# Kernel optimization log

Hardware: AMD Instinct MI355X
Metric: run time of the kernel (lower is better)

## Reference

```python
import jax, jax.numpy as jnp
import numpy as np

B, F, N = 128, 256, 2000

def setup_inputs() -> dict:
    key = jax.random.key(0)
    ks = jax.random.split(key, 10)
    s = 0.05
    return {
        'nfeature': jax.random.normal(ks[0], (B, F, N, 1), jnp.float32),
        'last_current': jax.random.randint(ks[1], (B, 2), 0, N, jnp.int32),
        'Wg': jax.random.normal(ks[2], (F, F), jnp.float32) * s,
        'bg': jax.random.normal(ks[3], (F,), jnp.float32) * s,
        'Wnode': jax.random.normal(ks[4], (3 * F, F), jnp.float32) * s,
        'bnode': jax.random.normal(ks[5], (3 * F,), jnp.float32) * s,
        'Wlc': jax.random.normal(ks[6], (F, 2 * F), jnp.float32) * s,
        'blc': jax.random.normal(ks[7], (F,), jnp.float32) * s,
        'Wproj': jax.random.normal(ks[8], (F, F), jnp.float32) * s,
        'bproj': jax.random.normal(ks[9], (F,), jnp.float32) * s,
    }

def reference(nfeature, last_current, Wg, bg, Wnode, bnode, Wlc, blc, Wproj, bproj):
    # nfeature: [B, F, N, 1]
    x = nfeature[..., 0]                                  # [B, F, N]
    f = x.shape[1]
    scale = 1.0 / jnp.sqrt(jnp.asarray(f, x.dtype))
    # global fixed query: max over nodes then Linear
    glb = jnp.max(x, axis=2)                              # [B, F]
    Q = glb @ Wg.T + bg                                   # [B, F]
    # node embeddings via 1x1 conv == channel GEMM, split into K, V, logit_K
    kvl = jnp.einsum('bfn,gf->bgn', x, Wnode) + bnode[None, :, None]  # [B, 3F, N]
    K, V, Klog = jnp.split(kvl, 3, axis=1)                # each [B, F, N]
    # gather last/current city features
    lc = jnp.take_along_axis(x, last_current[:, None, :], axis=2)     # [B, F, 2]
    context = jnp.concatenate([lc[:, :, 0], lc[:, :, 1]], axis=1)     # [B, 2F]
    cQ = context @ Wlc.T + blc + Q                        # [B, F]
    # attention: single query over N keys
    ucj = jnp.einsum('bf,bfn->bn', cQ, K) * scale         # [B, N]
    attn = jax.nn.softmax(ucj, axis=1)
    nc = jnp.einsum('bn,bfn->bf', attn, V)                # [B, F]
    nc = nc @ Wproj.T + bproj                             # [B, F]
    logits = jnp.einsum('bf,bfn->bn', nc, Klog) * scale   # [B, N]
    return jnp.tanh(logits) * 10.0
```

## Files before the change

### kernel.cpp

```cpp
#include <hip/hip_runtime.h>
#include <hip/hip_fp16.h>
#include <math.h>

#define BB 128
#define FF 256
#define NN 2000

typedef float f32x4 __attribute__((ext_vector_type(4)));
union H8 { f32x4 v; __half2 h[4]; };

__global__ __launch_bounds__(256) void k_convmax(const float* __restrict__ x,
                                                 __half* __restrict__ xh,
                                                 float* __restrict__ glb) {
    int row  = (blockIdx.x << 2) | (threadIdx.x >> 6);
    int lane = threadIdx.x & 63;
    const f32x4* src = (const f32x4*)(x + (size_t)row * NN);
    f32x4*       dst = (f32x4*)(xh + (size_t)row * NN);
    float m = -INFINITY;
    for (int i = lane; i < 250; i += 64) {
        f32x4 a = __builtin_nontemporal_load(src + 2 * i);
        f32x4 b = __builtin_nontemporal_load(src + 2 * i + 1);
        m = fmaxf(m, fmaxf(fmaxf(a.x, a.y), fmaxf(a.z, a.w)));
        m = fmaxf(m, fmaxf(fmaxf(b.x, b.y), fmaxf(b.z, b.w)));
        H8 o;
        o.h[0] = __floats2half2_rn(a.x, a.y);
        o.h[1] = __floats2half2_rn(a.z, a.w);
        o.h[2] = __floats2half2_rn(b.x, b.y);
        o.h[3] = __floats2half2_rn(b.z, b.w);
        dst[i] = o.v;
    }
#pragma unroll
    for (int off = 32; off; off >>= 1) m = fmaxf(m, __shfl_xor(m, off));
    if (!lane) glb[row] = m;
}

__global__ __launch_bounds__(256) void k_prep(
    const float* __restrict__ x, const int* __restrict__ lc,
    const float* __restrict__ glb,
    const float* __restrict__ Wg, const float* __restrict__ bg,
    const float* __restrict__ Wnode, const float* __restrict__ bnode,
    const float* __restrict__ Wlc, const float* __restrict__ blc,
    float* __restrict__ cK, float* __restrict__ cK0)
{
    int b = blockIdx.x;
    int f = threadIdx.x;
    __shared__ float s_glb[FF], s_ctx[2 * FF], s_cQ[FF], s_red[FF];
    const float* xb = x + (size_t)b * FF * NN;
    s_glb[f] = glb[b * FF + f];
    int l0 = lc[2 * b], l1 = lc[2 * b + 1];
    s_ctx[f]      = xb[(size_t)f * NN + l0];
    s_ctx[FF + f] = xb[(size_t)f * NN + l1];
    __syncthreads();
    const float* wg = Wg + (size_t)f * FF;
    float q0 = 0, q1 = 0, q2 = 0, q3 = 0;
    for (int j = 0; j < FF; j += 4) {
        q0 = fmaf(wg[j],     s_glb[j],     q0);
        q1 = fmaf(wg[j + 1], s_glb[j + 1], q1);
        q2 = fmaf(wg[j + 2], s_glb[j + 2], q2);
        q3 = fmaf(wg[j + 3], s_glb[j + 3], q3);
    }
    const float* wl = Wlc + (size_t)f * 2 * FF;
    for (int j = 0; j < 2 * FF; j += 4) {
        q0 = fmaf(wl[j],     s_ctx[j],     q0);
        q1 = fmaf(wl[j + 1], s_ctx[j + 1], q1);
        q2 = fmaf(wl[j + 2], s_ctx[j + 2], q2);
        q3 = fmaf(wl[j + 3], s_ctx[j + 3], q3);
    }
    float cq = bg[f] + blc[f] + ((q0 + q1) + (q2 + q3));
    s_cQ[f]  = cq;
    s_red[f] = cq * bnode[f];
    __syncthreads();
    float c0 = 0, c1 = 0;
    for (int g = 0; g < FF; g += 2) {
        c0 = fmaf(s_cQ[g],     Wnode[(size_t)g * FF + f],       c0);
        c1 = fmaf(s_cQ[g + 1], Wnode[(size_t)(g + 1) * FF + f], c1);
    }
    cK[b * FF + f] = c0 + c1;
    for (int s = 128; s > 0; s >>= 1) {
        if (f < s) s_red[f] += s_red[f + s];
        __syncthreads();
    }
    if (f == 0) cK0[b] = s_red[0];
}

__global__ __launch_bounds__(512) void k_attn(
    const __half* __restrict__ xh,
    const float* __restrict__ cK, const float* __restrict__ cK0,
    float* __restrict__ y_part8, float* __restrict__ m_part,
    float* __restrict__ s_part)
{
    int b = blockIdx.x >> 2, s = blockIdx.x & 3;
    int tid = threadIdx.x, w = tid >> 6, lane = tid & 63;
    __shared__ float s_cK[FF];
    __shared__ float s_buf[8][512];
    __shared__ float s_p[512];
    __shared__ float s_red[8], s_red2[8];
    if (tid < FF) s_cK[tid] = cK[b * FF + tid];
    __syncthreads();

    int n0 = s << 9;
    int nbase = n0 + (lane << 3);
    bool valid = nbase < NN;
    int cb = lane << 3;
    const __half* rp = xh + (size_t)(b * FF + (w << 5)) * NN + nbase;

    float a0 = 0, a1 = 0, a2 = 0, a3 = 0, a4 = 0, a5 = 0, a6 = 0, a7 = 0;
    if (valid) {
#pragma unroll
        for (int g = 0; g < 4; ++g) {
            f32x4 hv[8];
#pragma unroll
            for (int r = 0; r < 8; ++r)
                hv[r] = *(const f32x4*)(rp + (size_t)((g << 3) + r) * NN);
#pragma unroll
            for (int r = 0; r < 8; ++r) {
                H8 u; u.v = hv[r];
                float c = s_cK[(w << 5) + (g << 3) + r];
                float2 q0 = __half22float2(u.h[0]);
                float2 q1 = __half22float2(u.h[1]);
                float2 q2 = __half22float2(u.h[2]);
                float2 q3 = __half22float2(u.h[3]);
                a0 = fmaf(c, q0.x, a0); a1 = fmaf(c, q0.y, a1);
                a2 = fmaf(c, q1.x, a2); a3 = fmaf(c, q1.y, a3);
                a4 = fmaf(c, q2.x, a4); a5 = fmaf(c, q2.y, a5);
                a6 = fmaf(c, q3.x, a6); a7 = fmaf(c, q3.y, a7);
            }
        }
    }
    s_buf[w][cb + 0] = a0; s_buf[w][cb + 1] = a1;
    s_buf[w][cb + 2] = a2; s_buf[w][cb + 3] = a3;
    s_buf[w][cb + 4] = a4; s_buf[w][cb + 5] = a5;
    s_buf[w][cb + 6] = a6; s_buf[w][cb + 7] = a7;
    __syncthreads();

    const float scale = 0.0625f;
    float k0 = cK0[b];
    float u = 0.f;
#pragma unroll
    for (int ww = 0; ww < 8; ++ww) u += s_buf[ww][tid];
    float uu = (n0 + tid < NN) ? (u + k0) * scale : -INFINITY;
    float m = uu;
#pragma unroll
    for (int off = 32; off; off >>= 1) m = fmaxf(m, __shfl_xor(m, off));
    if (!lane) s_red[w] = m;
    __syncthreads();
    float M = s_red[0];
#pragma unroll
    for (int ww = 1; ww < 8; ++ww) M = fmaxf(M, s_red[ww]);
    float e = (uu > -INFINITY) ? __expf(uu - M) : 0.f;
    s_p[tid] = e;
    float ss = e;
#pragma unroll
    for (int off = 32; off; off >>= 1) ss += __shfl_xor(ss, off);
    if (!lane) s_red2[w] = ss;
    __syncthreads();
    if (!tid) {
        float S = 0.f;
#pragma unroll
        for (int ww = 0; ww < 8; ++ww) S += s_red2[ww];
        m_part[(b << 2) + s] = M;
        s_part[(b << 2) + s] = S;
    }

    float4 pa = *(const float4*)&s_p[cb];
    float4 pc = *(const float4*)&s_p[cb + 4];
    float* yout = y_part8 + (size_t)((b << 2) + s) * 2048 + (w << 8);
    int row = lane >> 3, k = lane & 7;
#pragma unroll
    for (int g = 0; g < 4; ++g) {
        float part[8];
#pragma unroll
        for (int r = 0; r < 8; ++r) {
            float acc = 0.f;
            if (valid) {
                H8 u2; u2.v = *(const f32x4*)(rp + (size_t)((g << 3) + r) * NN);
                float2 q0 = __half22float2(u2.h[0]);
                float2 q1 = __half22float2(u2.h[1]);
                float2 q2 = __half22float2(u2.h[2]);
                float2 q3 = __half22float2(u2.h[3]);
                acc = fmaf(pa.x, q0.x, acc); acc = fmaf(pa.y, q0.y, acc);
                acc = fmaf(pa.z, q1.x, acc); acc = fmaf(pa.w, q1.y, acc);
                acc = fmaf(pc.x, q2.x, acc); acc = fmaf(pc.y, q2.y, acc);
                acc = fmaf(pc.z, q3.x, acc); acc = fmaf(pc.w, q3.y, acc);
            }
            part[r] = acc;
        }
#pragma unroll
        for (int r = 0; r < 8; ++r) s_buf[w][(r << 6) + lane] = part[r];
        const float* srcp = &s_buf[w][(row << 6) + (k << 3)];
        float4 aa = *(const float4*)srcp;
        float4 bb = *(const float4*)(srcp + 4);
        yout[(g << 6) + lane] =
            ((aa.x + aa.y) + (aa.z + aa.w)) + ((bb.x + bb.y) + (bb.z + bb.w));
    }
}

__global__ __launch_bounds__(256) void k_dense(
    const float* __restrict__ y_part8, const float* __restrict__ m_part,
    const float* __restrict__ s_part,
    const float* __restrict__ Wnode, const float* __restrict__ bnode,
    const float* __restrict__ Wproj, const float* __restrict__ bproj,
    float* __restrict__ cL, float* __restrict__ cL0)
{
    int b = blockIdx.x;
    int f = threadIdx.x;
    int wid = f >> 6, lane = f & 63;
    __shared__ float s_y[FF], s_v[FF], s_red[4];

    float m0 = m_part[(b << 2)],     m1 = m_part[(b << 2) + 1];
    float m2 = m_part[(b << 2) + 2], m3 = m_part[(b << 2) + 3];
    float M = fmaxf(fmaxf(m0, m1), fmaxf(m2, m3));
    float w0 = __expf(m0 - M), w1 = __expf(m1 - M);
    float w2 = __expf(m2 - M), w3 = __expf(m3 - M);
    float S = s_part[(b << 2)] * w0 + s_part[(b << 2) + 1] * w1 +
              s_part[(b << 2) + 2] * w2 + s_part[(b << 2) + 3] * w3;
    float invS = 1.0f / S;
    const float* yb = y_part8 + ((size_t)b << 13);
    float wgt[4] = {w0, w1, w2, w3};
    float acc = 0.f;
#pragma unroll
    for (int s = 0; s < 4; ++s) {
        float4 aa = *(const float4*)(yb + (s << 11) + (f << 3));
        float4 bb = *(const float4*)(yb + (s << 11) + (f << 3) + 4);
        acc += wgt[s] * (((aa.x + aa.y) + (aa.z + aa.w)) + ((bb.x + bb.y) + (bb.z + bb.w)));
    }
    s_y[f] = acc * invS;
    __syncthreads();

    const float* wv = Wnode + (size_t)(FF + f) * FF;
    float a0 = 0, a1 = 0, a2 = 0, a3 = 0;
    for (int j = 0; j < FF; j += 4) {
        a0 = fmaf(wv[j],     s_y[j],     a0);
        a1 = fmaf(wv[j + 1], s_y[j + 1], a1);
        a2 = fmaf(wv[j + 2], s_y[j + 2], a2);
        a3 = fmaf(wv[j + 3], s_y[j + 3], a3);
    }
    s_v[f] = bnode[FF + f] + ((a0 + a1) + (a2 + a3));
    __syncthreads();
    const float* wp = Wproj + (size_t)f * FF;
    a0 = 0; a1 = 0; a2 = 0; a3 = 0;
    for (int j = 0; j < FF; j += 4) {
        a0 = fmaf(wp[j],     s_v[j],     a0);
        a1 = fmaf(wp[j + 1], s_v[j + 1], a1);
        a2 = fmaf(wp[j + 2], s_v[j + 2], a2);
        a3 = fmaf(wp[j + 3], s_v[j + 3], a3);
    }
    float nc2 = bproj[f] + ((a0 + a1) + (a2 + a3));
    __syncthreads();
    s_v[f] = nc2;
    __syncthreads();
    float c0 = 0, c1 = 0;
    for (int g = 0; g < FF; g += 2) {
        c0 = fmaf(s_v[g],     Wnode[(size_t)(2 * FF + g) * FF + f],     c0);
        c1 = fmaf(s_v[g + 1], Wnode[(size_t)(2 * FF + g + 1) * FF + f], c1);
    }
    cL[b * FF + f] = c0 + c1;
    float t = nc2 * bnode[2 * FF + f];
#pragma unroll
    for (int off = 32; off; off >>= 1) t += __shfl_xor(t, off);
    if (!lane) s_red[wid] = t;
    __syncthreads();
    if (!f) cL0[b] = s_red[0] + s_red[1] + s_red[2] + s_red[3];
}

__global__ __launch_bounds__(512) void k_logits(const __half* __restrict__ xh,
                                                const float* __restrict__ cL,
                                                const float* __restrict__ cL0,
                                                float* __restrict__ out)
{
    int b = blockIdx.x >> 2, s = blockIdx.x & 3;
    int tid = threadIdx.x, w = tid >> 6, lane = tid & 63;
    __shared__ float s_cL[FF];
    __shared__ float s_acc[8][512];
    if (tid < FF) s_cL[tid] = cL[b * FF + tid];
    __syncthreads();
    int n0 = s << 9;
    int nbase = n0 + (lane << 3);
    bool valid = nbase < NN;
    int cb = lane << 3;
    const __half* rp = xh + (size_t)(b * FF + (w << 5)) * NN + nbase;
    float a0 = 0, a1 = 0, a2 = 0, a3 = 0, a4 = 0, a5 = 0, a6 = 0, a7 = 0;
    if (valid) {
#pragma unroll
        for (int g = 0; g < 4; ++g) {
            f32x4 hv[8];
#pragma unroll
            for (int r = 0; r < 8; ++r)
                hv[r] = *(const f32x4*)(rp + (size_t)((g << 3) + r) * NN);
#pragma unroll
            for (int r = 0; r < 8; ++r) {
                H8 u; u.v = hv[r];
                float c = s_cL[(w << 5) + (g << 3) + r];
                float2 q0 = __half22float2(u.h[0]);
                float2 q1 = __half22float2(u.h[1]);
                float2 q2 = __half22float2(u.h[2]);
                float2 q3 = __half22float2(u.h[3]);
                a0 = fmaf(c, q0.x, a0); a1 = fmaf(c, q0.y, a1);
                a2 = fmaf(c, q1.x, a2); a3 = fmaf(c, q1.y, a3);
                a4 = fmaf(c, q2.x, a4); a5 = fmaf(c, q2.y, a5);
                a6 = fmaf(c, q3.x, a6); a7 = fmaf(c, q3.y, a7);
            }
        }
    }
    s_acc[w][cb + 0] = a0; s_acc[w][cb + 1] = a1;
    s_acc[w][cb + 2] = a2; s_acc[w][cb + 3] = a3;
    s_acc[w][cb + 4] = a4; s_acc[w][cb + 5] = a5;
    s_acc[w][cb + 6] = a6; s_acc[w][cb + 7] = a7;
    __syncthreads();
    int n = n0 + tid;
    if (n < NN) {
        float t = 0.f;
#pragma unroll
        for (int ww = 0; ww < 8; ++ww) t += s_acc[ww][tid];
        out[(size_t)b * NN + n] = tanhf((t + cL0[b]) * 0.0625f) * 10.f;
    }
}

extern "C" void kernel_launch(void* const* d_in, const int* in_sizes, int n_in,
                              void* d_out, int out_size, void* d_ws, size_t ws_size,
                              hipStream_t stream) {
    const float* x     = (const float*)d_in[0];
    const int*   lc    = (const int*)d_in[1];
    const float* Wg    = (const float*)d_in[2];
    const float* bg    = (const float*)d_in[3];
    const float* Wnode = (const float*)d_in[4];
    const float* bnode = (const float*)d_in[5];
    const float* Wlc   = (const float*)d_in[6];
    const float* blc   = (const float*)d_in[7];
    const float* Wproj = (const float*)d_in[8];
    const float* bproj = (const float*)d_in[9];
    float* out = (float*)d_out;

    float* ws      = (float*)d_ws;
    float* glb     = ws + 0;
    float* cK      = ws + 40960;
    float* cK0     = ws + 81920;
    float* m_part  = ws + 82432;
    float* s_part  = ws + 83456;
    float* cL      = ws + 84480;
    float* cL0     = ws + 117248;
    float* y_part8 = ws + 118272;
    __half* xh     = (__half*)(ws + (2 << 20));

    k_convmax<<<BB * FF / 4, 256, 0, stream>>>(x, xh, glb);
    k_prep   <<<BB, 256, 0, stream>>>(x, lc, glb, Wg, bg, Wnode, bnode, Wlc, blc, cK, cK0);
    k_attn   <<<BB * 4, 512, 0, stream>>>(xh, cK, cK0, y_part8, m_part, s_part);
    k_dense  <<<BB, 256, 0, stream>>>(y_part8, m_part, s_part, Wnode, bnode, Wproj, bproj, cL, cL0);
    k_logits <<<BB * 4, 512, 0, stream>>>(xh, cL, cL0, out);
}
```

Before: 196.1 us.

## Stage fp16 node tile in LDS so attention reads x once, split N into 8

The attention kernel now copies each block's fp16 feature tile (256 features x 256 nodes) into shared memory while it computes the scores. The weighted-V pass then reads that tile from LDS instead of reloading it from global memory, which removes the second global read. The node axis is split into 8 slices per batch instead of 4, giving more blocks. The partial outputs are reduced per slice into a compact y_part, and k_dense merges 8 partial softmax results. The cost is about 128KB of LDS per block, which limits occupancy, and a different thread-to-row mapping that adds a shuffle reduction.

```diff
diff --git a/kernel.cpp b/kernel.cpp
--- a/kernel.cpp
+++ b/kernel.cpp
@@ -5,6 +5,8 @@
 #define BB 128
 #define FF 256
 #define NN 2000
+#define SW 8
+#define SC 256
 
 typedef float f32x4 __attribute__((ext_vector_type(4)));
 union H8 { f32x4 v; __half2 h[4]; };
@@ -86,117 +88,129 @@
 __global__ __launch_bounds__(512) void k_attn(
     const __half* __restrict__ xh,
     const float* __restrict__ cK, const float* __restrict__ cK0,
-    float* __restrict__ y_part8, float* __restrict__ m_part,
+    float* __restrict__ y_part, float* __restrict__ m_part,
     float* __restrict__ s_part)
 {
-    int b = blockIdx.x >> 2, s = blockIdx.x & 3;
+    int b = blockIdx.x >> 3, st = blockIdx.x & 7;
     int tid = threadIdx.x, w = tid >> 6, lane = tid & 63;
+    int par = lane >> 5, chunk = lane & 31;
+    __shared__ __half tile[FF][SC];
+    __shared__ float s_u[8][SC];
+    __shared__ float s_p[SC];
     __shared__ float s_cK[FF];
-    __shared__ float s_buf[8][512];
-    __shared__ float s_p[512];
     __shared__ float s_red[8], s_red2[8];
     if (tid < FF) s_cK[tid] = cK[b * FF + tid];
     __syncthreads();
 
-    int n0 = s << 9;
-    int nbase = n0 + (lane << 3);
-    bool valid = nbase < NN;
-    int cb = lane << 3;
-    const __half* rp = xh + (size_t)(b * FF + (w << 5)) * NN + nbase;
-
-    float a0 = 0, a1 = 0, a2 = 0, a3 = 0, a4 = 0, a5 = 0, a6 = 0, a7 = 0;
-    if (valid) {
-#pragma unroll
-        for (int g = 0; g < 4; ++g) {
-            f32x4 hv[8];
-#pragma unroll
-            for (int r = 0; r < 8; ++r)
-                hv[r] = *(const f32x4*)(rp + (size_t)((g << 3) + r) * NN);
-#pragma unroll
-            for (int r = 0; r < 8; ++r) {
-                H8 u; u.v = hv[r];
-                float c = s_cK[(w << 5) + (g << 3) + r];
-                float2 q0 = __half22float2(u.h[0]);
-                float2 q1 = __half22float2(u.h[1]);
-                float2 q2 = __half22float2(u.h[2]);
-                float2 q3 = __half22float2(u.h[3]);
-                a0 = fmaf(c, q0.x, a0); a1 = fmaf(c, q0.y, a1);
-                a2 = fmaf(c, q1.x, a2); a3 = fmaf(c, q1.y, a3);
-                a4 = fmaf(c, q2.x, a4); a5 = fmaf(c, q2.y, a5);
-                a6 = fmaf(c, q3.x, a6); a7 = fmaf(c, q3.y, a7);
-            }
-        }
-    }
-    s_buf[w][cb + 0] = a0; s_buf[w][cb + 1] = a1;
-    s_buf[w][cb + 2] = a2; s_buf[w][cb + 3] = a3;
-    s_buf[w][cb + 4] = a4; s_buf[w][cb + 5] = a5;
-    s_buf[w][cb + 6] = a6; s_buf[w][cb + 7] = a7;
+    int colbase = (st << 8) + (chunk << 3);
+    bool cvalid = colbase < NN;
+    const __half* base = xh + ((size_t)(b * FF) + (w << 5) + par) * NN + colbase;
+
+    float up0 = 0, up1 = 0, up2 = 0, up3 = 0, up4 = 0, up5 = 0, up6 = 0, up7 = 0;
+#pragma unroll
+    for (int g = 0; g < 4; ++g) {
+        f32x4 hv[4];
+#pragma unroll
+        for (int r = 0; r < 4; ++r) {
+            if (cvalid) hv[r] = *(const f32x4*)(base + (size_t)((g << 3) + (r << 1)) * NN);
+            else        hv[r] = (f32x4){0.f, 0.f, 0.f, 0.f};
+        }
+#pragma unroll
+        for (int r = 0; r < 4; ++r) {
+            int row = (w << 5) + par + (g << 3) + (r << 1);
+            *(f32x4*)&tile[row][chunk << 3] = hv[r];
+            H8 u; u.v = hv[r];
+            float c = s_cK[row];
+            float2 q0 = __half22float2(u.h[0]);
+            float2 q1 = __half22float2(u.h[1]);
+            float2 q2 = __half22float2(u.h[2]);
+            float2 q3 = __half22float2(u.h[3]);
+            up0 = fmaf(c, q0.x, up0); up1 = fmaf(c, q0.y, up1);
+            up2 = fmaf(c, q1.x, up2); up3 = fmaf(c, q1.y, up3);
+            up4 = fmaf(c, q2.x, up4); up5 = fmaf(c, q2.y, up5);
+            up6 = fmaf(c, q3.x, up6); up7 = fmaf(c, q3.y, up7);
+        }
+    }
+    up0 += __shfl_xor(up0, 32); up1 += __shfl_xor(up1, 32);
+    up2 += __shfl_xor(up2, 32); up3 += __shfl_xor(up3, 32);
+    up4 += __shfl_xor(up4, 32); up5 += __shfl_xor(up5, 32);
+    up6 += __shfl_xor(up6, 32); up7 += __shfl_xor(up7, 32);
+    if (!par) {
+        f32x4 v0 = {up0, up1, up2, up3}, v1 = {up4, up5, up6, up7};
+        *(f32x4*)&s_u[w][chunk << 3]       = v0;
+        *(f32x4*)&s_u[w][(chunk << 3) + 4] = v1;
+    }
     __syncthreads();
 
     const float scale = 0.0625f;
-    float k0 = cK0[b];
-    float u = 0.f;
-#pragma unroll
-    for (int ww = 0; ww < 8; ++ww) u += s_buf[ww][tid];
-    float uu = (n0 + tid < NN) ? (u + k0) * scale : -INFINITY;
+    float uu = -INFINITY;
+    if (tid < SC) {
+        int col = (st << 8) + tid;
+        if (col < NN) {
+            float usum = 0.f;
+#pragma unroll
+            for (int ww = 0; ww < 8; ++ww) usum += s_u[ww][tid];
+            uu = (usum + cK0[b]) * scale;
+        }
+    }
     float m = uu;
 #pragma unroll
     for (int off = 32; off; off >>= 1) m = fmaxf(m, __shfl_xor(m, off));
-    if (!lane) s_red[w] = m;
-    __syncthreads();
-    float M = s_red[0];
-#pragma unroll
-    for (int ww = 1; ww < 8; ++ww) M = fmaxf(M, s_red[ww]);
+    if (!lane && w < 4) s_red[w] = m;
+    __syncthreads();
+    float M = fmaxf(fmaxf(s_red[0], s_red[1]), fmaxf(s_red[2], s_red[3]));
     float e = (uu > -INFINITY) ? __expf(uu - M) : 0.f;
-    s_p[tid] = e;
-    float ss = e;
-#pragma unroll
-    for (int off = 32; off; off >>= 1) ss += __shfl_xor(ss, off);
-    if (!lane) s_red2[w] = ss;
+    if (tid < SC) s_p[tid] = e;
+    float ssum = e;
+#pragma unroll
+    for (int off = 32; off; off >>= 1) ssum += __shfl_xor(ssum, off);
+    if (!lane && w < 4) s_red2[w] = ssum;
     __syncthreads();
     if (!tid) {
-        float S = 0.f;
-#pragma unroll
-        for (int ww = 0; ww < 8; ++ww) S += s_red2[ww];
-        m_part[(b << 2) + s] = M;
-        s_part[(b << 2) + s] = S;
-    }
-
-    float4 pa = *(const float4*)&s_p[cb];
-    float4 pc = *(const float4*)&s_p[cb + 4];
-    float* yout = y_part8 + (size_t)((b << 2) + s) * 2048 + (w << 8);
-    int row = lane >> 3, k = lane & 7;
-#pragma unroll
-    for (int g = 0; g < 4; ++g) {
-        float part[8];
-#pragma unroll
-        for (int r = 0; r < 8; ++r) {
-            float acc = 0.f;
-            if (valid) {
-                H8 u2; u2.v = *(const f32x4*)(rp + (size_t)((g << 3) + r) * NN);
-                float2 q0 = __half22float2(u2.h[0]);
-                float2 q1 = __half22float2(u2.h[1]);
-                float2 q2 = __half22float2(u2.h[2]);
-                float2 q3 = __half22float2(u2.h[3]);
-                acc = fmaf(pa.x, q0.x, acc); acc = fmaf(pa.y, q0.y, acc);
-                acc = fmaf(pa.z, q1.x, acc); acc = fmaf(pa.w, q1.y, acc);
-                acc = fmaf(pc.x, q2.x, acc); acc = fmaf(pc.y, q2.y, acc);
-                acc = fmaf(pc.z, q3.x, acc); acc = fmaf(pc.w, q3.y, acc);
-            }
-            part[r] = acc;
-        }
-#pragma unroll
-        for (int r = 0; r < 8; ++r) s_buf[w][(r << 6) + lane] = part[r];
-        const float* srcp = &s_buf[w][(row << 6) + (k << 3)];
-        float4 aa = *(const float4*)srcp;
-        float4 bb = *(const float4*)(srcp + 4);
-        yout[(g << 6) + lane] =
-            ((aa.x + aa.y) + (aa.z + aa.w)) + ((bb.x + bb.y) + (bb.z + bb.w));
+        m_part[(b << 3) + st] = M;
+        s_part[(b << 3) + st] = s_red2[0] + s_red2[1] + s_red2[2] + s_red2[3];
+    }
+
+    f32x4 pv0 = *(const f32x4*)&s_p[chunk << 3];
+    f32x4 pv1 = *(const f32x4*)&s_p[(chunk << 3) + 4];
+    float acc[16];
+#pragma unroll
+    for (int k = 0; k < 16; ++k) {
+        int row = (w << 5) + par + (k << 1);
+        H8 u; u.v = *(const f32x4*)&tile[row][chunk << 3];
+        float2 q0 = __half22float2(u.h[0]);
+        float2 q1 = __half22float2(u.h[1]);
+        float2 q2 = __half22float2(u.h[2]);
+        float2 q3 = __half22float2(u.h[3]);
+        float a = 0.f;
+        a = fmaf(pv0.x, q0.x, a); a = fmaf(pv0.y, q0.y, a);
+        a = fmaf(pv0.z, q1.x, a); a = fmaf(pv0.w, q1.y, a);
+        a = fmaf(pv1.x, q2.x, a); a = fmaf(pv1.y, q2.y, a);
+        a = fmaf(pv1.z, q3.x, a); a = fmaf(pv1.w, q3.y, a);
+        acc[k] = a;
+    }
+    __syncthreads();
+    float* tbuf = (float*)&tile[0][0];
+#pragma unroll
+    for (int k = 0; k < 16; ++k)
+        tbuf[(w << 10) + ((par + (k << 1)) << 5) + chunk] = acc[k];
+    __syncthreads();
+    {
+        int row = tid >> 1, half = tid & 1;
+        const float* src = tbuf + ((row >> 5) << 10) + ((row & 31) << 5) + (half << 4);
+        f32x4 a0 = *(const f32x4*)src;
+        f32x4 a1 = *(const f32x4*)(src + 4);
+        f32x4 a2 = *(const f32x4*)(src + 8);
+        f32x4 a3 = *(const f32x4*)(src + 12);
+        float sm = ((a0.x + a0.y) + (a0.z + a0.w)) + ((a1.x + a1.y) + (a1.z + a1.w)) +
+                   ((a2.x + a2.y) + (a2.z + a2.w)) + ((a3.x + a3.y) + (a3.z + a3.w));
+        sm += __shfl_xor(sm, 1);
+        if (!half) y_part[(size_t)((b << 3) + st) * FF + row] = sm;
     }
 }
 
 __global__ __launch_bounds__(256) void k_dense(
-    const float* __restrict__ y_part8, const float* __restrict__ m_part,
+    const float* __restrict__ y_part, const float* __restrict__ m_part,
     const float* __restrict__ s_part,
     const float* __restrict__ Wnode, const float* __restrict__ bnode,
     const float* __restrict__ Wproj, const float* __restrict__ bproj,
@@ -207,23 +221,20 @@
     int wid = f >> 6, lane = f & 63;
     __shared__ float s_y[FF], s_v[FF], s_red[4];
 
-    float m0 = m_part[(b << 2)],     m1 = m_part[(b << 2) + 1];
-    float m2 = m_part[(b << 2) + 2], m3 = m_part[(b << 2) + 3];
-    float M = fmaxf(fmaxf(m0, m1), fmaxf(m2, m3));
-    float w0 = __expf(m0 - M), w1 = __expf(m1 - M);
-    float w2 = __expf(m2 - M), w3 = __expf(m3 - M);
-    float S = s_part[(b << 2)] * w0 + s_part[(b << 2) + 1] * w1 +
-              s_part[(b << 2) + 2] * w2 + s_part[(b << 2) + 3] * w3;
+    float M = -INFINITY;
+#pragma unroll
+    for (int s = 0; s < 8; ++s) M = fmaxf(M, m_part[(b << 3) + s]);
+    float S = 0.f, wgt[8];
+#pragma unroll
+    for (int s = 0; s < 8; ++s) {
+        wgt[s] = __expf(m_part[(b << 3) + s] - M);
+        S = fmaf(wgt[s], s_part[(b << 3) + s], S);
+    }
     float invS = 1.0f / S;
-    const float* yb = y_part8 + ((size_t)b << 13);
-    float wgt[4] = {w0, w1, w2, w3};
     float acc = 0.f;
 #pragma unroll
-    for (int s = 0; s < 4; ++s) {
-        float4 aa = *(const float4*)(yb + (s << 11) + (f << 3));
-        float4 bb = *(const float4*)(yb + (s << 11) + (f << 3) + 4);
-        acc += wgt[s] * (((aa.x + aa.y) + (aa.z + aa.w)) + ((bb.x + bb.y) + (bb.z + bb.w)));
-    }
+    for (int s = 0; s < 8; ++s)
+        acc = fmaf(wgt[s], y_part[(size_t)((b << 3) + s) * FF + f], acc);
     s_y[f] = acc * invS;
     __syncthreads();
 
@@ -268,51 +279,59 @@
                                                 const float* __restrict__ cL0,
                                                 float* __restrict__ out)
 {
-    int b = blockIdx.x >> 2, s = blockIdx.x & 3;
+    int b = blockIdx.x >> 3, st = blockIdx.x & 7;
     int tid = threadIdx.x, w = tid >> 6, lane = tid & 63;
+    int par = lane >> 5, chunk = lane & 31;
     __shared__ float s_cL[FF];
-    __shared__ float s_acc[8][512];
+    __shared__ float s_acc[8][SC];
     if (tid < FF) s_cL[tid] = cL[b * FF + tid];
     __syncthreads();
-    int n0 = s << 9;
-    int nbase = n0 + (lane << 3);
-    bool valid = nbase < NN;
-    int cb = lane << 3;
-    const __half* rp = xh + (size_t)(b * FF + (w << 5)) * NN + nbase;
-    float a0 = 0, a1 = 0, a2 = 0, a3 = 0, a4 = 0, a5 = 0, a6 = 0, a7 = 0;
-    if (valid) {
+
+    int colbase = (st << 8) + (chunk << 3);
+    bool cvalid = colbase < NN;
+    const __half* base = xh + ((size_t)(b * FF) + (w << 5) + par) * NN + colbase;
+    float up0 = 0, up1 = 0, up2 = 0, up3 = 0, up4 = 0, up5 = 0, up6 = 0, up7 = 0;
+    if (cvalid) {
 #pragma unroll
         for (int g = 0; g < 4; ++g) {
-            f32x4 hv[8];
-#pragma unroll
-            for (int r = 0; r < 8; ++r)
-                hv[r] = *(const f32x4*)(rp + (size_t)((g << 3) + r) * NN);
-#pragma unroll
-            for (int r = 0; r < 8; ++r) {
+            f32x4 hv[4];
+#pragma unroll
+            for (int r = 0; r < 4; ++r)
+                hv[r] = *(const f32x4*)(base + (size_t)((g << 3) + (r << 1)) * NN);
+#pragma unroll
+            for (int r = 0; r < 4; ++r) {
+                int row = (w << 5) + par + (g << 3) + (r << 1);
                 H8 u; u.v = hv[r];
-                float c = s_cL[(w << 5) + (g << 3) + r];
+                float c = s_cL[row];
                 float2 q0 = __half22float2(u.h[0]);
                 float2 q1 = __half22float2(u.h[1]);
                 float2 q2 = __half22float2(u.h[2]);
                 float2 q3 = __half22float2(u.h[3]);
-                a0 = fmaf(c, q0.x, a0); a1 = fmaf(c, q0.y, a1);
-                a2 = fmaf(c, q1.x, a2); a3 = fmaf(c, q1.y, a3);
-                a4 = fmaf(c, q2.x, a4); a5 = fmaf(c, q2.y, a5);
-                a6 = fmaf(c, q3.x, a6); a7 = fmaf(c, q3.y, a7);
+                up0 = fmaf(c, q0.x, up0); up1 = fmaf(c, q0.y, up1);
+                up2 = fmaf(c, q1.x, up2); up3 = fmaf(c, q1.y, up3);
+                up4 = fmaf(c, q2.x, up4); up5 = fmaf(c, q2.y, up5);
+                up6 = fmaf(c, q3.x, up6); up7 = fmaf(c, q3.y, up7);
             }
         }
     }
-    s_acc[w][cb + 0] = a0; s_acc[w][cb + 1] = a1;
-    s_acc[w][cb + 2] = a2; s_acc[w][cb + 3] = a3;
-    s_acc[w][cb + 4] = a4; s_acc[w][cb + 5] = a5;
-    s_acc[w][cb + 6] = a6; s_acc[w][cb + 7] = a7;
-    __syncthreads();
-    int n = n0 + tid;
-    if (n < NN) {
-        float t = 0.f;
-#pragma unroll
-        for (int ww = 0; ww < 8; ++ww) t += s_acc[ww][tid];
-        out[(size_t)b * NN + n] = tanhf((t + cL0[b]) * 0.0625f) * 10.f;
+    up0 += __shfl_xor(up0, 32); up1 += __shfl_xor(up1, 32);
+    up2 += __shfl_xor(up2, 32); up3 += __shfl_xor(up3, 32);
+    up4 += __shfl_xor(up4, 32); up5 += __shfl_xor(up5, 32);
+    up6 += __shfl_xor(up6, 32); up7 += __shfl_xor(up7, 32);
+    if (!par) {
+        f32x4 v0 = {up0, up1, up2, up3}, v1 = {up4, up5, up6, up7};
+        *(f32x4*)&s_acc[w][chunk << 3]       = v0;
+        *(f32x4*)&s_acc[w][(chunk << 3) + 4] = v1;
+    }
+    __syncthreads();
+    if (tid < SC) {
+        int col = (st << 8) + tid;
+        if (col < NN) {
+            float t = 0.f;
+#pragma unroll
+            for (int ww = 0; ww < 8; ++ww) t += s_acc[ww][tid];
+            out[(size_t)b * NN + col] = tanhf((t + cL0[b]) * 0.0625f) * 10.f;
+        }
     }
 }
 
@@ -331,20 +350,20 @@
     const float* bproj = (const float*)d_in[9];
     float* out = (float*)d_out;
 
-    float* ws      = (float*)d_ws;
-    float* glb     = ws + 0;
-    float* cK      = ws + 40960;
-    float* cK0     = ws + 81920;
-    float* m_part  = ws + 82432;
-    float* s_part  = ws + 83456;
-    float* cL      = ws + 84480;
-    float* cL0     = ws + 117248;
-    float* y_part8 = ws + 118272;
-    __half* xh     = (__half*)(ws + (2 << 20));
+    float* ws     = (float*)d_ws;
+    float* glb    = ws + 0;
+    float* cK     = ws + 40960;
+    float* cK0    = ws + 81920;
+    float* m_part = ws + 82944;
+    float* s_part = ws + 84992;
+    float* cL     = ws + 87040;
+    float* cL0    = ws + 120832;
+    float* y_part = ws + 121856;
+    __half* xh    = (__half*)(ws + (2 << 20));
 
     k_convmax<<<BB * FF / 4, 256, 0, stream>>>(x, xh, glb);
     k_prep   <<<BB, 256, 0, stream>>>(x, lc, glb, Wg, bg, Wnode, bnode, Wlc, blc, cK, cK0);
-    k_attn   <<<BB * 4, 512, 0, stream>>>(xh, cK, cK0, y_part8, m_part, s_part);
-    k_dense  <<<BB, 256, 0, stream>>>(y_part8, m_part, s_part, Wnode, bnode, Wproj, bproj, cL, cL0);
-    k_logits <<<BB * 4, 512, 0, stream>>>(xh, cL, cL0, out);
-}
+    k_attn   <<<BB * SW, 512, 0, stream>>>(xh, cK, cK0, y_part, m_part, s_part);
+    k_dense  <<<BB, 256, 0, stream>>>(y_part, m_part, s_part, Wnode, bnode, Wproj, bproj, cL, cL0);
+    k_logits <<<BB * SW, 512, 0, stream>>>(xh, cL, cL0, out);
+}
```

Measured after the change: 191.5 us. 2.4% less time.
